# Optimization experiments

Measured on AMD Instinct MI355X. Metric: run time of the kernel, lower is better.

## Reference

```python
import jax, jax.numpy as jnp
import numpy as np

N_NODES = 50000
N_EDGES = 600000
IN_FEATS = 16
H_FEAT = 128
N_CLASSES = 4
N_HIDDEN_LAYERS = 19  # conv2..conv20


def setup_inputs() -> dict:
    key = jax.random.key(0)
    ks = jax.random.split(key, 10)
    x = jax.random.normal(ks[0], (N_NODES, IN_FEATS), dtype=jnp.float32)
    edge_index = jax.random.randint(ks[1], (2, N_EDGES), 0, N_NODES, dtype=jnp.int32)
    edge_attr = jax.random.uniform(ks[2], (N_EDGES, 1), dtype=jnp.float32)
    s_in = 1.0 / np.sqrt(IN_FEATS)
    s_h = 1.0 / np.sqrt(H_FEAT)
    W_in = jax.random.uniform(ks[3], (IN_FEATS, H_FEAT), minval=-s_in, maxval=s_in, dtype=jnp.float32)
    b_in = jax.random.uniform(ks[4], (H_FEAT,), minval=-s_in, maxval=s_in, dtype=jnp.float32)
    W_h = jax.random.uniform(ks[5], (N_HIDDEN_LAYERS, H_FEAT, H_FEAT), minval=-s_h, maxval=s_h, dtype=jnp.float32)
    b_h = jax.random.uniform(ks[6], (N_HIDDEN_LAYERS, H_FEAT), minval=-s_h, maxval=s_h, dtype=jnp.float32)
    W_fc = jax.random.uniform(ks[7], (H_FEAT, N_CLASSES), minval=-s_h, maxval=s_h, dtype=jnp.float32)
    b_fc = jax.random.uniform(ks[8], (N_CLASSES,), minval=-s_h, maxval=s_h, dtype=jnp.float32)
    return {"x": x, "edge_index": edge_index, "edge_attr": edge_attr,
            "W_in": W_in, "b_in": b_in, "W_h": W_h, "b_h": b_h,
            "W_fc": W_fc, "b_fc": b_fc}


def reference(x, edge_index, edge_attr, W_in, b_in, W_h, b_h, W_fc, b_fc):
    src, dst = edge_index[0], edge_index[1]
    ew = edge_attr[:, 0]  # edge_weight = edge_attr[:, 0]
    n = x.shape[0]
    # degree by dst, clamped at 1
    deg = jax.ops.segment_sum(jnp.ones(src.shape[0], dtype=x.dtype), dst, num_segments=n)
    deg_inv = 1.0 / jnp.maximum(deg, 1.0)  # [N]

    def conv(h, W, b):
        h = h @ W + b                       # [N, out]
        msg = h[src] * ew[:, None]          # [E, out]
        agg = jax.ops.segment_sum(msg, dst, num_segments=n)
        return agg * deg_inv[:, None]

    h = jax.nn.leaky_relu(conv(x, W_in, b_in))

    def step(h, params):
        W, b = params
        return jax.nn.leaky_relu(conv(h, W, b)), None

    h, _ = jax.lax.scan(step, h, (W_h, b_h))
    return h @ W_fc + b_fc  # [N, num_classes]
```

## Files before the change

kernel.cpp:

```cpp
#include <hip/hip_runtime.h>
#include <hip/hip_fp16.h>

#define N_NODES 50000
#define N_EDGES 600000
#define IN_F 16
#define HF 128
#define NC 4
#define NHL 19
#define N_FP8_LAYERS 18
#define WS_STRIDE 136

__device__ __forceinline__ float lrelu(float x) { return x > 0.f ? x : 0.01f * x; }

struct h4 { __half2 a, b; };

typedef _Float16 f16;
typedef _Float16 f16x8 __attribute__((ext_vector_type(8)));
typedef float    f32x4 __attribute__((ext_vector_type(4)));
typedef float    f32x2 __attribute__((ext_vector_type(2)));

__device__ __forceinline__ unsigned pack_fp8x4(float a, float b, float c, float d) {
    int r = __builtin_amdgcn_cvt_pk_fp8_f32(a, b, 0, false);
    r = __builtin_amdgcn_cvt_pk_fp8_f32(c, d, r, true);
    return (unsigned)r;
}


__global__ void count_deg_k(const int* __restrict__ dst, int* __restrict__ cnt) {
    int e = blockIdx.x * 256 + threadIdx.x;
    if (e < N_EDGES) atomicAdd(&cnt[dst[e]], 1);
}

__global__ void scan_k(const int* __restrict__ cnt, int* __restrict__ rowptr,
                       float* __restrict__ dinv) {
    __shared__ int wsum[16];
    __shared__ int carry_s;
    int t = threadIdx.x;
    int lane = t & 63, wid = t >> 6;
    if (t == 0) carry_s = 0;
    __syncthreads();
    for (int base = 0; base < N_NODES; base += 4096) {
        int idx = base + t * 4;
        int4 v = make_int4(0, 0, 0, 0);
        if (idx + 3 < N_NODES) v = *(const int4*)&cnt[idx];
        else {
            if (idx     < N_NODES) v.x = cnt[idx];
            if (idx + 1 < N_NODES) v.y = cnt[idx + 1];
            if (idx + 2 < N_NODES) v.z = cnt[idx + 2];
            if (idx + 3 < N_NODES) v.w = cnt[idx + 3];
        }
        if (idx + 3 < N_NODES) {
            float4 dv = make_float4(1.f / fmaxf((float)v.x, 1.f), 1.f / fmaxf((float)v.y, 1.f),
                                    1.f / fmaxf((float)v.z, 1.f), 1.f / fmaxf((float)v.w, 1.f));
            *(float4*)&dinv[idx] = dv;
        } else {
            if (idx     < N_NODES) dinv[idx]     = 1.f / fmaxf((float)v.x, 1.f);
            if (idx + 1 < N_NODES) dinv[idx + 1] = 1.f / fmaxf((float)v.y, 1.f);
            if (idx + 2 < N_NODES) dinv[idx + 2] = 1.f / fmaxf((float)v.z, 1.f);
            if (idx + 3 < N_NODES) dinv[idx + 3] = 1.f / fmaxf((float)v.w, 1.f);
        }
        int s1 = v.x + v.y, s2 = s1 + v.z, total = s2 + v.w;
        int sc = total;
#pragma unroll
        for (int off = 1; off < 64; off <<= 1) {
            int u = __shfl_up(sc, off, 64);
            if (lane >= off) sc += u;
        }
        if (lane == 63) wsum[wid] = sc;
        __syncthreads();
        if (t < 16) {
            int w = wsum[t];
#pragma unroll
            for (int off = 1; off < 16; off <<= 1) {
                int u = __shfl_up(w, off, 64);
                if (t >= off) w += u;
            }
            wsum[t] = w;
        }
        __syncthreads();
        int prefix = carry_s + (wid > 0 ? wsum[wid - 1] : 0) + (sc - total);
        if (idx     < N_NODES) rowptr[idx]     = prefix;
        if (idx + 1 < N_NODES) rowptr[idx + 1] = prefix + v.x;
        if (idx + 2 < N_NODES) rowptr[idx + 2] = prefix + s1;
        if (idx + 3 < N_NODES) rowptr[idx + 3] = prefix + s2;
        __syncthreads();
        if (t == 0) carry_s += wsum[15];
        __syncthreads();
    }
    if (t == 0) rowptr[N_NODES] = carry_s;
}

__global__ void fill_k(const int* __restrict__ src, const int* __restrict__ dst,
                       const float* __restrict__ ea, const int* __restrict__ rowptr,
                       int* __restrict__ fill, int2* __restrict__ edg,
                       const float* __restrict__ dinv) {
    int e = blockIdx.x * 256 + threadIdx.x;
    if (e < N_EDGES) {
        int d = dst[e];
        int pos = rowptr[d] + atomicAdd(&fill[d], 1);
        edg[pos] = make_int2(src[e], __float_as_int(ea[e] * dinv[d]));
    }
}


__global__ void wconv_k(const float* __restrict__ Wh, __half* __restrict__ Wt) {
    int idx = blockIdx.x * 256 + threadIdx.x;
    if (idx >= NHL * HF * HF) return;
    int l = idx / (HF * HF);
    int r = idx - l * (HF * HF);
    int n = r >> 7;
    int k = r & 127;
    Wt[idx] = __float2half(Wh[(size_t)l * HF * HF + k * HF + n]);
}


__global__ void gemm_in_k(const float* __restrict__ X, const float* __restrict__ W,
                          const float* __restrict__ b, unsigned* __restrict__ T8) {
    __shared__ float Ws[IN_F * HF];
    int t = threadIdx.x;
    ((float4*)Ws)[t]       = ((const float4*)W)[t];
    ((float4*)Ws)[t + 256] = ((const float4*)W)[t + 256];
    __syncthreads();
    int row = blockIdx.x * 16 + (t >> 4);
    if (row >= N_NODES) return;
    int tx = t & 15;
    int c0 = tx * 4, c1 = 64 + tx * 4;
    float4 a0 = *(const float4*)&b[c0];
    float4 a1 = *(const float4*)&b[c1];
    const float4* xr = (const float4*)(X + row * IN_F);
#pragma unroll
    for (int k4 = 0; k4 < 4; k4++) {
        float4 xv = xr[k4];
        const float* xp = (const float*)&xv;
#pragma unroll
        for (int kk = 0; kk < 4; kk++) {
            int k = k4 * 4 + kk;
            float4 w0 = *(const float4*)&Ws[k * HF + c0];
            float4 w1 = *(const float4*)&Ws[k * HF + c1];
            float xs = xp[kk];
            a0.x = fmaf(xs, w0.x, a0.x); a0.y = fmaf(xs, w0.y, a0.y);
            a0.z = fmaf(xs, w0.z, a0.z); a0.w = fmaf(xs, w0.w, a0.w);
            a1.x = fmaf(xs, w1.x, a1.x); a1.y = fmaf(xs, w1.y, a1.y);
            a1.z = fmaf(xs, w1.z, a1.z); a1.w = fmaf(xs, w1.w, a1.w);
        }
    }
    T8[(size_t)row * 32 + tx]      = pack_fp8x4(a0.x, a0.y, a0.z, a0.w);
    T8[(size_t)row * 32 + 16 + tx] = pack_fp8x4(a1.x, a1.y, a1.z, a1.w);
}


template <bool FP8IN, bool FP8OUT>
__global__ __launch_bounds__(256) void gemm_mfma_k(const void* __restrict__ Hin,
                                                   const __half* __restrict__ Wt,
                                                   const float* __restrict__ b,
                                                   void* __restrict__ Tout) {
    __shared__ __half Ws[HF * WS_STRIDE];
    __shared__ __half Hs[64 * WS_STRIDE];
    int t = threadIdx.x;
    int rbase = blockIdx.x * 64;
    int u16 = t & 15;
    int rg  = t >> 4;

#pragma unroll
    for (int p = 0; p < 8; p++) {
        int n = p * 16 + rg;
        *(float4*)&Ws[n * WS_STRIDE + u16 * 8] = *(const float4*)&Wt[(size_t)n * HF + u16 * 8];
    }
#pragma unroll
    for (int p = 0; p < 4; p++) {
        int rl = p * 16 + rg;
        int row = rbase + rl;
        if (row >= N_NODES) row = N_NODES - 1;
        if (FP8IN) {
            uint2 hv8 = *(const uint2*)&((const unsigned char*)Hin)[(size_t)row * HF + u16 * 8];
            f32x2 a0 = __builtin_amdgcn_cvt_pk_f32_fp8((int)hv8.x, false);
            f32x2 a1 = __builtin_amdgcn_cvt_pk_f32_fp8((int)hv8.x, true);
            f32x2 a2 = __builtin_amdgcn_cvt_pk_f32_fp8((int)hv8.y, false);
            f32x2 a3 = __builtin_amdgcn_cvt_pk_f32_fp8((int)hv8.y, true);
            h4 o0, o1;
            o0.a = __floats2half2_rn(a0.x, a0.y); o0.b = __floats2half2_rn(a1.x, a1.y);
            o1.a = __floats2half2_rn(a2.x, a2.y); o1.b = __floats2half2_rn(a3.x, a3.y);
            float4 pk;
            ((h4*)&pk)[0] = o0;
            *(h4*)((char*)&pk + 8) = o1;
            *(float4*)&Hs[rl * WS_STRIDE + u16 * 8] = pk;
        } else {
            *(float4*)&Hs[rl * WS_STRIDE + u16 * 8] =
                *(const float4*)&((const __half*)Hin)[(size_t)row * HF + u16 * 8];
        }
    }
    __syncthreads();

    int lane = t & 63;
    int w    = t >> 6;
    int wr   = w * 16;
    int m16  = lane & 15;
    int q    = lane >> 4;

    f16x8 af[4];
#pragma unroll
    for (int kc = 0; kc < 4; kc++)
        af[kc] = *(const f16x8*)&Hs[(wr + m16) * WS_STRIDE + kc * 32 + q * 8];

    f32x4 acc[8];
#pragma unroll
    for (int nt = 0; nt < 8; nt++) {
        float bv = b[nt * 16 + m16];
        acc[nt] = (f32x4){bv, bv, bv, bv};
#pragma unroll
        for (int kc = 0; kc < 4; kc++) {
            f16x8 bf = *(const f16x8*)&Ws[(nt * 16 + m16) * WS_STRIDE + kc * 32 + q * 8];
            acc[nt] = __builtin_amdgcn_mfma_f32_16x16x32_f16(af[kc], bf, acc[nt], 0, 0, 0);
        }
    }
    __syncthreads();

#pragma unroll
    for (int nt = 0; nt < 8; nt++)
#pragma unroll
        for (int r = 0; r < 4; r++)
            Hs[(wr + q * 4 + r) * WS_STRIDE + nt * 16 + m16] = __float2half(acc[nt][r]);
    __syncthreads();

#pragma unroll
    for (int p = 0; p < 4; p++) {
        int rl = p * 16 + rg;
        int row = rbase + rl;
        if (row < N_NODES) {
            float4 cv = *(float4*)&Hs[rl * WS_STRIDE + u16 * 8];
            if (FP8OUT) {
                __half2* hp = (__half2*)&cv;
                float2 f0 = __half22float2(hp[0]);
                float2 f1 = __half22float2(hp[1]);
                float2 f2 = __half22float2(hp[2]);
                float2 f3 = __half22float2(hp[3]);
                uint2 o;
                o.x = pack_fp8x4(f0.x, f0.y, f1.x, f1.y);
                o.y = pack_fp8x4(f2.x, f2.y, f3.x, f3.y);
                *(uint2*)&((unsigned char*)Tout)[(size_t)row * HF + u16 * 8] = o;
            } else {
                *(float4*)&((__half*)Tout)[(size_t)row * HF + u16 * 8] = cv;
            }
        }
    }
}


template <bool FP8IN, bool FP8OUT>
__global__ __launch_bounds__(256) void agg4_k(const void* __restrict__ Tin,
                                              void* __restrict__ O,
                                              const int* __restrict__ rowptr,
                                              const int2* __restrict__ edg) {
    int gw = blockIdx.x * 4 + (threadIdx.x >> 6);
    int v0 = gw * 4;
    if (v0 >= N_NODES) return;
    int lane = threadIdx.x & 63;
    int q  = lane >> 4;
    int li = lane & 15;

    int rp = rowptr[v0 + min(lane, 4)];
    int r0 = __shfl(rp, 0, 64), r1 = __shfl(rp, 1, 64), r2 = __shfl(rp, 2, 64);
    int r3 = __shfl(rp, 3, 64), r4 = __shfl(rp, 4, 64);
    int e0 = __shfl(rp, q, 64);
    int e1 = __shfl(rp, q + 1, 64);
    int degmax = max(max(r1 - r0, r2 - r1), max(r3 - r2, r4 - r3));
    int nb = (degmax + 15) >> 4;

    const uint2* T8  = (const uint2*)Tin;
    const uint4* T16 = (const uint4*)Tin;

    float acc[8] = {0.f, 0.f, 0.f, 0.f, 0.f, 0.f, 0.f, 0.f};

    for (int eb = 0; eb < nb; eb++) {
        int idx = e0 + eb * 16 + li;
        bool ok = idx < e1;
        int2 rec = edg[ok ? idx : 0];
        if (!ok) rec.y = 0;
        int sb = q << 4;
#pragma unroll
        for (int g = 0; g < 2; g++) {
            int   ss[8];
            float ww[8];
#pragma unroll
            for (int u = 0; u < 8; u++) {
                int sl = sb + g * 8 + u;
                ss[u] = __shfl(rec.x, sl, 64);
                ww[u] = __int_as_float(__shfl(rec.y, sl, 64));
            }
            if (FP8IN) {
                uint2 gv[8];
#pragma unroll
                for (int u = 0; u < 8; u++)
                    gv[u] = T8[(size_t)ss[u] * 16 + li];
#pragma unroll
                for (int u = 0; u < 8; u++) {
                    f32x2 p0 = __builtin_amdgcn_cvt_pk_f32_fp8((int)gv[u].x, false);
                    f32x2 p1 = __builtin_amdgcn_cvt_pk_f32_fp8((int)gv[u].x, true);
                    f32x2 p2 = __builtin_amdgcn_cvt_pk_f32_fp8((int)gv[u].y, false);
                    f32x2 p3 = __builtin_amdgcn_cvt_pk_f32_fp8((int)gv[u].y, true);
                    acc[0] = fmaf(p0.x, ww[u], acc[0]);
                    acc[1] = fmaf(p0.y, ww[u], acc[1]);
                    acc[2] = fmaf(p1.x, ww[u], acc[2]);
                    acc[3] = fmaf(p1.y, ww[u], acc[3]);
                    acc[4] = fmaf(p2.x, ww[u], acc[4]);
                    acc[5] = fmaf(p2.y, ww[u], acc[5]);
                    acc[6] = fmaf(p3.x, ww[u], acc[6]);
                    acc[7] = fmaf(p3.y, ww[u], acc[7]);
                }
            } else {
                uint4 gv[8];
#pragma unroll
                for (int u = 0; u < 8; u++)
                    gv[u] = T16[(size_t)ss[u] * 16 + li];
#pragma unroll
                for (int u = 0; u < 8; u++) {
                    __half2* hp = (__half2*)&gv[u];
                    float2 p0 = __half22float2(hp[0]);
                    float2 p1 = __half22float2(hp[1]);
                    float2 p2 = __half22float2(hp[2]);
                    float2 p3 = __half22float2(hp[3]);
                    acc[0] = fmaf(p0.x, ww[u], acc[0]);
                    acc[1] = fmaf(p0.y, ww[u], acc[1]);
                    acc[2] = fmaf(p1.x, ww[u], acc[2]);
                    acc[3] = fmaf(p1.y, ww[u], acc[3]);
                    acc[4] = fmaf(p2.x, ww[u], acc[4]);
                    acc[5] = fmaf(p2.y, ww[u], acc[5]);
                    acc[6] = fmaf(p3.x, ww[u], acc[6]);
                    acc[7] = fmaf(p3.y, ww[u], acc[7]);
                }
            }
        }
    }
    int v = v0 + q;
    if (FP8OUT) {
        uint2 o;
        o.x = pack_fp8x4(lrelu(acc[0]), lrelu(acc[1]), lrelu(acc[2]), lrelu(acc[3]));
        o.y = pack_fp8x4(lrelu(acc[4]), lrelu(acc[5]), lrelu(acc[6]), lrelu(acc[7]));
        ((uint2*)O)[(size_t)v * 16 + li] = o;
    } else {
        h4 oa, ob;
        oa.a = __floats2half2_rn(lrelu(acc[0]), lrelu(acc[1]));
        oa.b = __floats2half2_rn(lrelu(acc[2]), lrelu(acc[3]));
        ob.a = __floats2half2_rn(lrelu(acc[4]), lrelu(acc[5]));
        ob.b = __floats2half2_rn(lrelu(acc[6]), lrelu(acc[7]));
        uint4 ov;
        ((h4*)&ov)[0] = oa;
        *(h4*)((char*)&ov + 8) = ob;
        ((uint4*)O)[(size_t)v * 16 + li] = ov;
    }
}


__global__ void fc_k(const __half* __restrict__ H, const float* __restrict__ W,
                     const float* __restrict__ b, float* __restrict__ out) {
    int r = blockIdx.x * 256 + threadIdx.x;
    if (r >= N_NODES) return;
    float4 acc = *(const float4*)b;
    const h4* hp = (const h4*)(H + (size_t)r * HF);
    const float4* w4 = (const float4*)W;
#pragma unroll
    for (int k4 = 0; k4 < 32; k4++) {
        h4 hh = hp[k4];
        float2 p0 = __half22float2(hh.a);
        float2 p1 = __half22float2(hh.b);
        float4 wa = w4[k4 * 4 + 0], wb = w4[k4 * 4 + 1];
        float4 wc = w4[k4 * 4 + 2], wd = w4[k4 * 4 + 3];
        acc.x = fmaf(p0.x, wa.x, acc.x); acc.y = fmaf(p0.x, wa.y, acc.y);
        acc.z = fmaf(p0.x, wa.z, acc.z); acc.w = fmaf(p0.x, wa.w, acc.w);
        acc.x = fmaf(p0.y, wb.x, acc.x); acc.y = fmaf(p0.y, wb.y, acc.y);
        acc.z = fmaf(p0.y, wb.z, acc.z); acc.w = fmaf(p0.y, wb.w, acc.w);
        acc.x = fmaf(p1.x, wc.x, acc.x); acc.y = fmaf(p1.x, wc.y, acc.y);
        acc.z = fmaf(p1.x, wc.z, acc.z); acc.w = fmaf(p1.x, wc.w, acc.w);
        acc.x = fmaf(p1.y, wd.x, acc.x); acc.y = fmaf(p1.y, wd.y, acc.y);
        acc.z = fmaf(p1.y, wd.z, acc.z); acc.w = fmaf(p1.y, wd.w, acc.w);
    }
    *(float4*)&out[r * NC] = acc;
}


extern "C" void kernel_launch(void* const* d_in, const int* in_sizes, int n_in,
                              void* d_out, int out_size, void* d_ws, size_t ws_size,
                              hipStream_t stream) {
    const float* X   = (const float*)d_in[0];
    const int*   EI  = (const int*)d_in[1];
    const float* EA  = (const float*)d_in[2];
    const float* Win = (const float*)d_in[3];
    const float* bin = (const float*)d_in[4];
    const float* Wh  = (const float*)d_in[5];
    const float* bh  = (const float*)d_in[6];
    const float* Wfc = (const float*)d_in[7];
    const float* bfc = (const float*)d_in[8];
    float* out = (float*)d_out;
    const int* src = EI;
    const int* dst = EI + N_EDGES;

    char* ws = (char*)d_ws;
    size_t off = 0;
    void*   O   = (void*)(ws + off);   off += (size_t)N_NODES * HF * 2;
    void*   T   = (void*)(ws + off);   off += (size_t)N_NODES * HF * 2;
    __half* Wt  = (__half*)(ws + off); off += (size_t)NHL * HF * HF * 2;
    int2* edg   = (int2*)(ws + off);  off += (size_t)N_EDGES * 8;
    int* rowptr = (int*)(ws + off);   off += (((size_t)(N_NODES + 1) * 4 + 15) / 16) * 16;
    int* cnt    = (int*)(ws + off);   off += (size_t)N_NODES * 4;
    int* fill   = (int*)(ws + off);   off += (size_t)N_NODES * 4;
    float* dinv = (float*)(ws + off); off += (size_t)N_NODES * 4;

    hipMemsetAsync(cnt, 0, N_NODES * 4, stream);
    hipMemsetAsync(fill, 0, N_NODES * 4, stream);
    count_deg_k<<<(N_EDGES + 255) / 256, 256, 0, stream>>>(dst, cnt);
    scan_k<<<1, 1024, 0, stream>>>(cnt, rowptr, dinv);
    fill_k<<<(N_EDGES + 255) / 256, 256, 0, stream>>>(src, dst, EA, rowptr, fill, edg, dinv);
    wconv_k<<<(NHL * HF * HF + 255) / 256, 256, 0, stream>>>(Wh, Wt);

    const int aggg  = (N_NODES / 4 + 3) / 4;
    const int gemmg = (N_NODES + 63) / 64;

    gemm_in_k<<<(N_NODES + 15) / 16, 256, 0, stream>>>(X, Win, bin, (unsigned*)T);
    agg4_k<true, true><<<aggg, 256, 0, stream>>>(T, O, rowptr, edg);
    for (int l = 0; l < N_FP8_LAYERS; l++) {
        gemm_mfma_k<true, true><<<gemmg, 256, 0, stream>>>(
            O, Wt + (size_t)l * HF * HF, bh + (size_t)l * HF, T);
        if (l < N_FP8_LAYERS - 1)
            agg4_k<true, true><<<aggg, 256, 0, stream>>>(T, O, rowptr, edg);
        else
            agg4_k<true, false><<<aggg, 256, 0, stream>>>(T, O, rowptr, edg);
    }
    for (int l = N_FP8_LAYERS; l < NHL; l++) {
        gemm_mfma_k<false, false><<<gemmg, 256, 0, stream>>>(
            O, Wt + (size_t)l * HF * HF, bh + (size_t)l * HF, T);
        agg4_k<false, false><<<aggg, 256, 0, stream>>>(T, O, rowptr, edg);
    }
    fc_k<<<(N_NODES + 255) / 256, 256, 0, stream>>>((const __half*)O, Wfc, bfc, out);
}
```

Before: 697.3 us.

## Pack edge records into 32 bits and use FP8 MFMA GEMM for early layers

Edge records are packed into one 32-bit word: a 16-bit source index and an fp16 normalized weight. This halves the edge-list traffic read by every aggregation pass. A new GEMM kernel uses fp8 weights and the 16x16x32 fp8 MFMA, with the output staged through LDS, for the first 17 hidden layers instead of the fp16 MFMA path. The cost is lower precision in both the weights and the edge weights, and the packing assumes fewer than 65536 nodes.

New measurement: 712.6 us. 1.02x slower.

```diff
diff --git a/kernel.cpp b/kernel.cpp
--- a/kernel.cpp
+++ b/kernel.cpp
@@ -7,8 +7,8 @@
 #define HF 128
 #define NC 4
 #define NHL 19
-#define N_FP8_LAYERS 18
 #define WS_STRIDE 136
+#define W8_STRIDE 136
 
 __device__ __forceinline__ float lrelu(float x) { return x > 0.f ? x : 0.01f * x; }
 
@@ -92,13 +92,15 @@
 
 __global__ void fill_k(const int* __restrict__ src, const int* __restrict__ dst,
                        const float* __restrict__ ea, const int* __restrict__ rowptr,
-                       int* __restrict__ fill, int2* __restrict__ edg,
+                       int* __restrict__ fill, unsigned* __restrict__ edg,
                        const float* __restrict__ dinv) {
     int e = blockIdx.x * 256 + threadIdx.x;
     if (e < N_EDGES) {
         int d = dst[e];
+        float w = ea[e] * dinv[d];
         int pos = rowptr[d] + atomicAdd(&fill[d], 1);
-        edg[pos] = make_int2(src[e], __float_as_int(ea[e] * dinv[d]));
+        unsigned hw = (unsigned)__half_as_ushort(__float2half(w));
+        edg[pos] = (unsigned)src[e] | (hw << 16);
     }
 }
 
@@ -111,6 +113,18 @@
     int n = r >> 7;
     int k = r & 127;
     Wt[idx] = __float2half(Wh[(size_t)l * HF * HF + k * HF + n]);
+}
+
+__global__ void wconv8_k(const float* __restrict__ Wh, unsigned* __restrict__ W8) {
+    int idx = blockIdx.x * 256 + threadIdx.x;
+    if (idx >= NHL * HF * HF / 4) return;
+    int l = idx / (HF * HF / 4);
+    int r = idx - l * (HF * HF / 4);
+    int n  = r >> 5;
+    int k4 = (r & 31) * 4;
+    const float* Wl = Wh + (size_t)l * HF * HF;
+    W8[idx] = pack_fp8x4(Wl[(k4 + 0) * HF + n], Wl[(k4 + 1) * HF + n],
+                         Wl[(k4 + 2) * HF + n], Wl[(k4 + 3) * HF + n]);
 }
 
 
@@ -146,6 +160,75 @@
     }
     T8[(size_t)row * 32 + tx]      = pack_fp8x4(a0.x, a0.y, a0.z, a0.w);
     T8[(size_t)row * 32 + 16 + tx] = pack_fp8x4(a1.x, a1.y, a1.z, a1.w);
+}
+
+
+__global__ __launch_bounds__(256) void gemm8_k(const unsigned char* __restrict__ H8,
+                                               const unsigned char* __restrict__ W8,
+                                               const float* __restrict__ b,
+                                               unsigned char* __restrict__ T8) {
+    __shared__ unsigned char Ws8[HF * W8_STRIDE];
+    __shared__ unsigned char Hs8[64 * W8_STRIDE];
+    int t = threadIdx.x;
+    int rbase = blockIdx.x * 64;
+    int u16 = t & 15;
+    int rg  = t >> 4;
+
+#pragma unroll
+    for (int p = 0; p < 8; p++) {
+        int n = p * 16 + rg;
+        *(uint2*)&Ws8[n * W8_STRIDE + u16 * 8] = *(const uint2*)&W8[(size_t)n * HF + u16 * 8];
+    }
+#pragma unroll
+    for (int p = 0; p < 4; p++) {
+        int rl = p * 16 + rg;
+        int row = rbase + rl;
+        if (row >= N_NODES) row = N_NODES - 1;
+        *(uint2*)&Hs8[rl * W8_STRIDE + u16 * 8] = *(const uint2*)&H8[(size_t)row * HF + u16 * 8];
+    }
+    __syncthreads();
+
+    int lane = t & 63;
+    int w    = t >> 6;
+    int wr   = w * 16;
+    int m16  = lane & 15;
+    int q    = lane >> 4;
+
+    long af[4];
+#pragma unroll
+    for (int kc = 0; kc < 4; kc++)
+        af[kc] = *(const long*)&Hs8[(wr + m16) * W8_STRIDE + kc * 32 + q * 8];
+
+    f32x4 acc[8];
+#pragma unroll
+    for (int nt = 0; nt < 8; nt++) {
+        float bv = b[nt * 16 + m16];
+        acc[nt] = (f32x4){bv, bv, bv, bv};
+#pragma unroll
+        for (int kc = 0; kc < 4; kc++) {
+            long bf = *(const long*)&Ws8[(nt * 16 + m16) * W8_STRIDE + kc * 32 + q * 8];
+            acc[nt] = __builtin_amdgcn_mfma_f32_16x16x32_fp8_fp8(af[kc], bf, acc[nt], 0, 0, 0);
+        }
+    }
+    __syncthreads();
+
+#pragma unroll
+    for (int nt = 0; nt < 8; nt++)
+#pragma unroll
+        for (int r = 0; r < 4; r++) {
+            float v = lrelu(acc[nt][r]) == 0.f ? acc[nt][r] : acc[nt][r];
+            Hs8[(wr + q * 4 + r) * W8_STRIDE + nt * 16 + m16] =
+                (unsigned char)(__builtin_amdgcn_cvt_pk_fp8_f32(v, v, 0, false) & 0xFF);
+        }
+    __syncthreads();
+
+#pragma unroll
+    for (int p = 0; p < 4; p++) {
+        int rl = p * 16 + rg;
+        int row = rbase + rl;
+        if (row < N_NODES)
+            *(uint2*)&T8[(size_t)row * HF + u16 * 8] = *(uint2*)&Hs8[rl * W8_STRIDE + u16 * 8];
+    }
 }
 
 
@@ -250,7 +333,7 @@
 __global__ __launch_bounds__(256) void agg4_k(const void* __restrict__ Tin,
                                               void* __restrict__ O,
                                               const int* __restrict__ rowptr,
-                                              const int2* __restrict__ edg) {
+                                              const unsigned* __restrict__ edg) {
     int gw = blockIdx.x * 4 + (threadIdx.x >> 6);
     int v0 = gw * 4;
     if (v0 >= N_NODES) return;
@@ -274,8 +357,8 @@
     for (int eb = 0; eb < nb; eb++) {
         int idx = e0 + eb * 16 + li;
         bool ok = idx < e1;
-        int2 rec = edg[ok ? idx : 0];
-        if (!ok) rec.y = 0;
+        unsigned rec = edg[ok ? idx : 0];
+        if (!ok) rec &= 0xFFFFu;
         int sb = q << 4;
 #pragma unroll
         for (int g = 0; g < 2; g++) {
@@ -283,9 +366,9 @@
             float ww[8];
 #pragma unroll
             for (int u = 0; u < 8; u++) {
-                int sl = sb + g * 8 + u;
-                ss[u] = __shfl(rec.x, sl, 64);
-                ww[u] = __int_as_float(__shfl(rec.y, sl, 64));
+                int rv = __shfl((int)rec, sb + g * 8 + u, 64);
+                ss[u] = rv & 0xFFFF;
+                ww[u] = __half2float(__ushort_as_half((unsigned short)((unsigned)rv >> 16)));
             }
             if (FP8IN) {
                 uint2 gv[8];
@@ -396,10 +479,11 @@
 
     char* ws = (char*)d_ws;
     size_t off = 0;
-    void*   O   = (void*)(ws + off);   off += (size_t)N_NODES * HF * 2;
-    void*   T   = (void*)(ws + off);   off += (size_t)N_NODES * HF * 2;
-    __half* Wt  = (__half*)(ws + off); off += (size_t)NHL * HF * HF * 2;
-    int2* edg   = (int2*)(ws + off);  off += (size_t)N_EDGES * 8;
+    void*     O    = (void*)(ws + off);     off += (size_t)N_NODES * HF * 2;
+    void*     T    = (void*)(ws + off);     off += (size_t)N_NODES * HF * 2;
+    __half*   Wt   = (__half*)(ws + off);   off += (size_t)NHL * HF * HF * 2;
+    unsigned* W8   = (unsigned*)(ws + off); off += (size_t)NHL * HF * HF;
+    unsigned* edg  = (unsigned*)(ws + off); off += (size_t)N_EDGES * 4;
     int* rowptr = (int*)(ws + off);   off += (((size_t)(N_NODES + 1) * 4 + 15) / 16) * 16;
     int* cnt    = (int*)(ws + off);   off += (size_t)N_NODES * 4;
     int* fill   = (int*)(ws + off);   off += (size_t)N_NODES * 4;
@@ -411,24 +495,24 @@
     scan_k<<<1, 1024, 0, stream>>>(cnt, rowptr, dinv);
     fill_k<<<(N_EDGES + 255) / 256, 256, 0, stream>>>(src, dst, EA, rowptr, fill, edg, dinv);
     wconv_k<<<(NHL * HF * HF + 255) / 256, 256, 0, stream>>>(Wh, Wt);
+    wconv8_k<<<(NHL * HF * HF / 4 + 255) / 256, 256, 0, stream>>>(Wh, W8);
 
     const int aggg  = (N_NODES / 4 + 3) / 4;
     const int gemmg = (N_NODES + 63) / 64;
 
     gemm_in_k<<<(N_NODES + 15) / 16, 256, 0, stream>>>(X, Win, bin, (unsigned*)T);
     agg4_k<true, true><<<aggg, 256, 0, stream>>>(T, O, rowptr, edg);
-    for (int l = 0; l < N_FP8_LAYERS; l++) {
-        gemm_mfma_k<true, true><<<gemmg, 256, 0, stream>>>(
-            O, Wt + (size_t)l * HF * HF, bh + (size_t)l * HF, T);
-        if (l < N_FP8_LAYERS - 1)
-            agg4_k<true, true><<<aggg, 256, 0, stream>>>(T, O, rowptr, edg);
-        else
-            agg4_k<true, false><<<aggg, 256, 0, stream>>>(T, O, rowptr, edg);
-    }
-    for (int l = N_FP8_LAYERS; l < NHL; l++) {
-        gemm_mfma_k<false, false><<<gemmg, 256, 0, stream>>>(
-            O, Wt + (size_t)l * HF * HF, bh + (size_t)l * HF, T);
-        agg4_k<false, false><<<aggg, 256, 0, stream>>>(T, O, rowptr, edg);
-    }
+    for (int l = 0; l < 17; l++) {
+        gemm8_k<<<gemmg, 256, 0, stream>>>(
+            (const unsigned char*)O, (const unsigned char*)(W8 + (size_t)l * HF * HF / 4),
+            bh + (size_t)l * HF, (unsigned char*)T);
+        agg4_k<true, true><<<aggg, 256, 0, stream>>>(T, O, rowptr, edg);
+    }
+    gemm_mfma_k<true, true><<<gemmg, 256, 0, stream>>>(
+        O, Wt + (size_t)17 * HF * HF, bh + (size_t)17 * HF, T);
+    agg4_k<true, false><<<aggg, 256, 0, stream>>>(T, O, rowptr, edg);
+    gemm_mfma_k<false, false><<<gemmg, 256, 0, stream>>>(
+        O, Wt + (size_t)18 * HF * HF, bh + (size_t)18 * HF, T);
+    agg4_k<false, false><<<aggg, 256, 0, stream>>>(T, O, rowptr, edg);
     fc_k<<<(N_NODES + 255) / 256, 256, 0, stream>>>((const __half*)O, Wfc, bfc, out);
 }
```
